# Performance work log

Hardware: AMD Instinct MI355X
Metric: run time of the kernel (lower is better)

## Reference

```python
import jax, jax.numpy as jnp
import numpy as np

B, N, L, D = 4, 2048, 12, 128  # batch, nodes, in_len, d_model


def _glorot(key, shape):
    fan_in = shape[0]
    return jax.random.normal(key, shape, dtype=jnp.float32) / jnp.sqrt(jnp.float32(fan_in))


def setup_inputs() -> dict:
    key = jax.random.key(0)
    ks = jax.random.split(key, 12)
    x = jax.random.normal(ks[0], (B, N, L, D), dtype=jnp.float32)
    adj = jax.random.uniform(ks[1], (N, N), dtype=jnp.float32)  # dense weighted adjacency
    # mlp2: Linear(L*D -> D)
    W_mlp2 = _glorot(ks[2], (L * D, D)); b_mlp2 = jnp.zeros((D,), jnp.float32)
    # GNN: three DenseSAGEConv layers (lin_rel on aggregated, lin_root on self)
    Wr1 = _glorot(ks[3], (D, D)); Wo1 = _glorot(ks[4], (D, D)); b1 = jnp.zeros((D,), jnp.float32)
    Wr2 = _glorot(ks[5], (D, D)); Wo2 = _glorot(ks[6], (D, D)); b2 = jnp.zeros((D,), jnp.float32)
    Wr3 = _glorot(ks[7], (D, D)); Wo3 = _glorot(ks[8], (D, D)); b3 = jnp.zeros((D,), jnp.float32)
    # mlp1: Linear(D -> L*D)
    W_mlp1 = _glorot(ks[9], (D, L * D)); b_mlp1 = jnp.zeros((L * D,), jnp.float32)
    return {"x": x, "adj": adj, "W_mlp2": W_mlp2, "b_mlp2": b_mlp2,
            "Wr1": Wr1, "Wo1": Wo1, "b1": b1,
            "Wr2": Wr2, "Wo2": Wo2, "b2": b2,
            "Wr3": Wr3, "Wo3": Wo3, "b3": b3,
            "W_mlp1": W_mlp1, "b_mlp1": b_mlp1}


def reference(x, adj, W_mlp2, b_mlp2, Wr1, Wo1, b1, Wr2, Wo2, b2, Wr3, Wo3, b3, W_mlp1, b_mlp1):
    b_, n_, l_, d_ = x.shape
    xf = x.reshape(b_, n_, l_ * d_)                      # 'b n l d -> b n (l d)'
    h = xf @ W_mlp2 + b_mlp2                             # mlp2: (B,N,D)
    deg = jnp.clip(adj.sum(axis=-1, keepdims=True), 1.0, None)  # (N,1)

    def sage(hin, Wr, Wo, bb):
        # mean neighbor aggregation: (adj @ h) / deg, then rel + root linear
        agg = jnp.einsum('mn,bnd->bmd', adj, hin) / deg
        return agg @ Wr + hin @ Wo + bb

    h = jax.nn.relu(sage(h, Wr1, Wo1, b1))
    h = jax.nn.relu(sage(h, Wr2, Wo2, b2))
    h = sage(h, Wr3, Wo3, b3)                            # gnn1_embed output (B,N,D)
    out = h @ W_mlp1 + b_mlp1                            # mlp1: (B,N,L*D)
    return out
```

## Files before the change

### kernel.cpp

```cpp
#include <hip/hip_runtime.h>

typedef __attribute__((ext_vector_type(8))) short short8;
typedef __attribute__((ext_vector_type(4))) short short4v;
typedef __attribute__((ext_vector_type(4))) float floatx4;

__device__ inline short to_bf16s(float f) {
    unsigned u = __builtin_bit_cast(unsigned, f);
    unsigned r = u + 0x7FFFu + ((u >> 16) & 1u);
    return (short)(r >> 16);
}

__device__ inline void dma16(const short* g, short* l) {
    __builtin_amdgcn_global_load_lds(
        (const __attribute__((address_space(1))) unsigned int*)(const void*)g,
        (__attribute__((address_space(3))) unsigned int*)(void*)l,
        16, 0, 0);
}

template <typename T> struct Ld8;
template <> struct Ld8<short> {
    static __device__ inline short8 load(const short* p) { return *(const short8*)p; }
};
template <> struct Ld8<float> {
    static __device__ inline short8 load(const float* p) {
        float4 f0 = *(const float4*)p;
        float4 f1 = *(const float4*)(p + 4);
        short8 r;
        r[0] = to_bf16s(f0.x); r[1] = to_bf16s(f0.y);
        r[2] = to_bf16s(f0.z); r[3] = to_bf16s(f0.w);
        r[4] = to_bf16s(f1.x); r[5] = to_bf16s(f1.y);
        r[6] = to_bf16s(f1.z); r[7] = to_bf16s(f1.w);
        return r;
    }
};

struct PrepArgs {
    const float* adj;
    const float* W2; const float* W1;
    const float* Wr0; const float* Wo0;
    const float* Wr1; const float* Wo1;
    const float* Wr2; const float* Wo2;
    short* adjS; short* W2T; short* W1T;
    short* BigB0; short* BigB1; short* BigB2;
};

__global__ __launch_bounds__(256) void prep(PrepArgs p) {
    int bid = blockIdx.x;
    if (bid < 2048) {
        const float* src = p.adj + (size_t)bid * 2048;
        float s = 0.f;
        for (int c = threadIdx.x; c < 2048; c += 256) s += src[c];
        __shared__ float red[256];
        red[threadIdx.x] = s;
        __syncthreads();
        for (int st = 128; st > 0; st >>= 1) {
            if (threadIdx.x < st) red[threadIdx.x] += red[threadIdx.x + st];
            __syncthreads();
        }
        float d = red[0];
        d = d < 1.f ? 1.f : d;
        float inv = 1.f / d;
        short* dst = p.adjS + (size_t)bid * 2048;
        for (int c = threadIdx.x; c < 2048; c += 256) dst[c] = to_bf16s(src[c] * inv);
        return;
    }
    int t = bid - 2048;
    __shared__ short tile[32][33];
    int tx = threadIdx.x & 31, ty0 = threadIdx.x >> 5;
    const float* in; int C_; int bx, by;
    short* outp; int outld, copies, copystride, outofs;
    if (t < 192) {
        bx = (t & 3) * 32; by = (t >> 2) * 32; in = p.W2; C_ = 128;
        outp = p.W2T; outld = 1536; copies = 1; copystride = 0; outofs = 0;
    } else if (t < 384) {
        int u = t - 192; bx = (u % 48) * 32; by = (u / 48) * 32; in = p.W1; C_ = 1536;
        outp = p.W1T; outld = 128; copies = 1; copystride = 0; outofs = 0;
    } else {
        int u = t - 384; int l = u / 32; int v = u % 32;
        const float* Wr[3] = {p.Wr0, p.Wr1, p.Wr2};
        const float* Wo[3] = {p.Wo0, p.Wo1, p.Wo2};
        short* BB[3] = {p.BigB0, p.BigB1, p.BigB2};
        outp = BB[l]; outld = 640; C_ = 128;
        if (v < 16) { in = Wr[l]; bx = (v & 3) * 32; by = (v >> 2) * 32;
                      copies = 4; copystride = 128; outofs = 0; }
        else { v -= 16; in = Wo[l]; bx = (v & 3) * 32; by = (v >> 2) * 32;
               copies = 1; copystride = 0; outofs = 512; }
    }
    for (int i = ty0; i < 32; i += 8)
        tile[i][tx] = to_bf16s(in[(size_t)(by + i) * C_ + bx + tx]);
    __syncthreads();
    for (int i = ty0; i < 32; i += 8) {
        short v = tile[tx][i];
        for (int c = 0; c < copies; ++c)
            outp[(size_t)(bx + i) * outld + (by + tx) + outofs + c * copystride] = v;
    }
}

#define LDSTR 72

template <typename TA, int RELU, int ROWMAP, int HTW>
__global__ __launch_bounds__(256) void gemmT(
    const TA* __restrict__ A, int lda,
    const short* __restrict__ B, int ldb, int kTiles,
    const float* __restrict__ bias,
    short* __restrict__ C, int ldc, int colofs,
    short* __restrict__ HT) {
    __shared__ __align__(16) short lds[2 * 96 * LDSTR];

    int tid = threadIdx.x;
    int blockM = blockIdx.x * 32;
    int blockN = blockIdx.y * 64;

    int srow = tid >> 3;
    int scol = (tid & 7) * 8;

    const TA* Abase = A + (size_t)blockM * lda;
    const short* Bbase = B + (size_t)blockN * ldb;

    short8 a0_  = Ld8<TA>::load(Abase + (size_t)srow * lda + scol);
    short8 b00_ = Ld8<short>::load(Bbase + (size_t)srow * ldb + scol);
    short8 b10_ = Ld8<short>::load(Bbase + (size_t)(srow + 32) * ldb + scol);
    short8 a1_  = Ld8<TA>::load(Abase + (size_t)srow * lda + 64 + scol);
    short8 b01_ = Ld8<short>::load(Bbase + (size_t)srow * ldb + 64 + scol);
    short8 b11_ = Ld8<short>::load(Bbase + (size_t)(srow + 32) * ldb + 64 + scol);

    floatx4 acc[2];
    #pragma unroll
    for (int j = 0; j < 2; ++j)
        #pragma unroll
        for (int r = 0; r < 4; ++r) acc[j][r] = 0.f;

    int lane = tid & 63;
    int w = tid >> 6;
    int wr = w >> 1, wc = w & 1;
    int quad = lane >> 4, l15 = lane & 15;

    short* buf0 = lds;
    short* buf1 = lds + 96 * LDSTR;

    for (int it = 0; it < kTiles; it += 2) {
        *(short8*)(buf0 + srow * LDSTR + scol) = a0_;
        *(short8*)(buf0 + (32 + srow) * LDSTR + scol) = b00_;
        *(short8*)(buf0 + (64 + srow) * LDSTR + scol) = b10_;
        asm volatile("s_waitcnt lgkmcnt(0)" ::: "memory");
        __builtin_amdgcn_s_barrier();
        if (it + 2 < kTiles) {
            int ko = (it + 2) * 64;
            a0_  = Ld8<TA>::load(Abase + (size_t)srow * lda + ko + scol);
            b00_ = Ld8<short>::load(Bbase + (size_t)srow * ldb + ko + scol);
            b10_ = Ld8<short>::load(Bbase + (size_t)(srow + 32) * ldb + ko + scol);
        }
        {
            const short* Arow = buf0 + (wr * 16 + l15) * LDSTR;
            const short* Brow = buf0 + (32 + wc * 32 + l15) * LDSTR;
            #pragma unroll
            for (int ks = 0; ks < 2; ++ks) {
                int kof = ks * 32 + quad * 8;
                short8 a0 = *(const short8*)(Arow + kof);
                short8 b0 = *(const short8*)(Brow + kof);
                short8 b1 = *(const short8*)(Brow + 16 * LDSTR + kof);
                acc[0] = __builtin_amdgcn_mfma_f32_16x16x32_bf16(a0, b0, acc[0], 0, 0, 0);
                acc[1] = __builtin_amdgcn_mfma_f32_16x16x32_bf16(a0, b1, acc[1], 0, 0, 0);
            }
        }
        *(short8*)(buf1 + srow * LDSTR + scol) = a1_;
        *(short8*)(buf1 + (32 + srow) * LDSTR + scol) = b01_;
        *(short8*)(buf1 + (64 + srow) * LDSTR + scol) = b11_;
        asm volatile("s_waitcnt lgkmcnt(0)" ::: "memory");
        __builtin_amdgcn_s_barrier();
        if (it + 3 < kTiles) {
            int ko = (it + 3) * 64;
            a1_  = Ld8<TA>::load(Abase + (size_t)srow * lda + ko + scol);
            b01_ = Ld8<short>::load(Bbase + (size_t)srow * ldb + ko + scol);
            b11_ = Ld8<short>::load(Bbase + (size_t)(srow + 32) * ldb + ko + scol);
        }
        {
            const short* Arow = buf1 + (wr * 16 + l15) * LDSTR;
            const short* Brow = buf1 + (32 + wc * 32 + l15) * LDSTR;
            #pragma unroll
            for (int ks = 0; ks < 2; ++ks) {
                int kof = ks * 32 + quad * 8;
                short8 a0 = *(const short8*)(Arow + kof);
                short8 b0 = *(const short8*)(Brow + kof);
                short8 b1 = *(const short8*)(Brow + 16 * LDSTR + kof);
                acc[0] = __builtin_amdgcn_mfma_f32_16x16x32_bf16(a0, b0, acc[0], 0, 0, 0);
                acc[1] = __builtin_amdgcn_mfma_f32_16x16x32_bf16(a0, b1, acc[1], 0, 0, 0);
            }
        }
    }

    #pragma unroll
    for (int tj = 0; tj < 2; ++tj) {
        int col = blockN + wc * 32 + tj * 16 + l15;
        float bv = bias[col];
        int m0 = blockM + wr * 16 + quad * 4;
        short4v pk;
        #pragma unroll
        for (int r = 0; r < 4; ++r) {
            int m = m0 + r;
            float xv = acc[tj][r] + bv;
            if (RELU) xv = xv > 0.f ? xv : 0.f;
            short v = to_bf16s(xv);
            pk[r] = v;
            int orow = ROWMAP ? (((m & 2047) << 2) | (m >> 11)) : m;
            C[(size_t)orow * ldc + col + colofs] = v;
            if (HTW && !ROWMAP) {
                HT[(size_t)((m & 3) * 128 + col) * 2048 + (m >> 2)] = v;
            }
        }
        if (HTW && ROWMAP) {
            int b = m0 >> 11, n0 = m0 & 2047;
            *(short4v*)(HT + (size_t)(b * 128 + col) * 2048 + n0) = pk;
        }
    }
}

__global__ __launch_bounds__(256) void gemmS(const short* __restrict__ A,
                                             const short* __restrict__ B,
                                             short* __restrict__ C) {
    __shared__ __align__(16) short lds3[3 * 12288];

    int tid = threadIdx.x;
    int kz = blockIdx.z * 512;

    int kswz = (((tid & 7) ^ ((tid >> 3) & 7))) * 8;
    const short* Ab = A + (size_t)(blockIdx.x * 64 + (tid >> 3)) * 2048 + kz + kswz;
    const short* Bb = B + (size_t)(blockIdx.y * 128 + (tid >> 3)) * 2048 + kz + kswz;

    floatx4 acc[2][4];
    #pragma unroll
    for (int i = 0; i < 2; ++i)
        #pragma unroll
        for (int j = 0; j < 4; ++j)
            #pragma unroll
            for (int r = 0; r < 4; ++r) acc[i][j][r] = 0.f;

    int lane = tid & 63;
    int w = tid >> 6;
    int wr = w >> 1, wc = w & 1;
    int quad = lane >> 4, l15 = lane & 15;

    auto stage = [&](int slot, int it) {
        short* As = lds3 + slot * 12288;
        short* Bs = As + 4096;
        const short* Ag = Ab + it * 64;
        const short* Bg = Bb + it * 64;
        dma16(Ag, As + tid * 8);
        dma16(Ag + (size_t)32 * 2048, As + tid * 8 + 2048);
        #pragma unroll
        for (int r = 0; r < 4; ++r)
            dma16(Bg + (size_t)r * 32 * 2048, Bs + tid * 8 + r * 2048);
    };

    stage(0, 0);
    stage(1, 1);

    int slot = 0;
    for (int it = 0; it < 8; ++it) {
        if (it < 7) asm volatile("s_waitcnt vmcnt(6)" ::: "memory");
        else        asm volatile("s_waitcnt vmcnt(0)" ::: "memory");
        __builtin_amdgcn_s_barrier();
        if (it + 2 < 8) {
            int s2 = slot + 2; if (s2 >= 3) s2 -= 3;
            stage(s2, it + 2);
        }
        const short* As = lds3 + slot * 12288;
        const short* Bs = As + 4096;
        #pragma unroll
        for (int ks = 0; ks < 2; ++ks) {
            int cswz = (((ks * 4 + quad) ^ (l15 & 7))) * 8;
            short8 af[2], bfr[4];
            #pragma unroll
            for (int i = 0; i < 2; ++i)
                af[i] = *(const short8*)(As + (wr * 32 + i * 16 + l15) * 64 + cswz);
            #pragma unroll
            for (int j = 0; j < 4; ++j)
                bfr[j] = *(const short8*)(Bs + (wc * 64 + j * 16 + l15) * 64 + cswz);
            #pragma unroll
            for (int i = 0; i < 2; ++i)
                #pragma unroll
                for (int j = 0; j < 4; ++j)
                    acc[i][j] = __builtin_amdgcn_mfma_f32_16x16x32_bf16(af[i], bfr[j], acc[i][j], 0, 0, 0);
        }
        slot = (slot + 1 == 3) ? 0 : slot + 1;
    }

    int colofs = blockIdx.z * 128;
    #pragma unroll
    for (int ti = 0; ti < 2; ++ti) {
        #pragma unroll
        for (int tj = 0; tj < 4; ++tj) {
            int j = blockIdx.y * 128 + wc * 64 + tj * 16 + l15;
            int jhi = j >> 7, jlo = j & 127;
            int row0 = blockIdx.x * 64 + wr * 32 + ti * 16 + quad * 4;
            #pragma unroll
            for (int r = 0; r < 4; ++r) {
                int m = row0 + r;
                C[(size_t)(m * 4 + jhi) * 640 + jlo + colofs] = to_bf16s(acc[ti][tj][r]);
            }
        }
    }
}

__global__ __launch_bounds__(256) void gemmL(
    const short* __restrict__ A, int lda,
    const short* __restrict__ B, int ldb,
    int kChunkIters, const float* __restrict__ bias,
    float* __restrict__ Cf, int ldc) {
    __shared__ __align__(16) short As[128 * 64];
    __shared__ __align__(16) short Bs[128 * 64];

    int tid = threadIdx.x;
    int blockM = blockIdx.x * 128;
    int blockN = blockIdx.y * 128;

    int kswz = (((tid & 7) ^ ((tid >> 3) & 7))) * 8;
    const short* Ab = A + (size_t)(blockM + (tid >> 3)) * lda + kswz;
    const short* Bb = B + (size_t)(blockN + (tid >> 3)) * ldb + kswz;
    short* Al = As + tid * 8;
    short* Bl = Bs + tid * 8;

    floatx4 acc[4][4];
    #pragma unroll
    for (int i = 0; i < 4; ++i)
        #pragma unroll
        for (int j = 0; j < 4; ++j)
            #pragma unroll
            for (int r = 0; r < 4; ++r) acc[i][j][r] = 0.f;

    int lane = tid & 63;
    int w = tid >> 6;
    int wr = w >> 1, wc = w & 1;
    int quad = lane >> 4, l15 = lane & 15;

    for (int it = 0; it < kChunkIters; ++it) {
        const short* Ag = Ab + it * 64;
        const short* Bg = Bb + it * 64;
        #pragma unroll
        for (int r = 0; r < 4; ++r) {
            dma16(Ag + (size_t)r * 32 * lda, Al + r * 2048);
            dma16(Bg + (size_t)r * 32 * ldb, Bl + r * 2048);
        }
        __syncthreads();
        #pragma unroll
        for (int ks = 0; ks < 2; ++ks) {
            int cswz = (((ks * 4 + quad) ^ (l15 & 7))) * 8;
            short8 af[4], bfr[4];
            #pragma unroll
            for (int i = 0; i < 4; ++i)
                af[i] = *(const short8*)(As + (wr * 64 + i * 16 + l15) * 64 + cswz);
            #pragma unroll
            for (int j = 0; j < 4; ++j)
                bfr[j] = *(const short8*)(Bs + (wc * 64 + j * 16 + l15) * 64 + cswz);
            #pragma unroll
            for (int i = 0; i < 4; ++i)
                #pragma unroll
                for (int j = 0; j < 4; ++j)
                    acc[i][j] = __builtin_amdgcn_mfma_f32_16x16x32_bf16(af[i], bfr[j], acc[i][j], 0, 0, 0);
        }
        __syncthreads();
    }

    #pragma unroll
    for (int ti = 0; ti < 4; ++ti) {
        #pragma unroll
        for (int tj = 0; tj < 4; ++tj) {
            int col = blockN + wc * 64 + tj * 16 + l15;
            float bv = bias[col];
            int row0 = blockM + wr * 64 + ti * 16 + quad * 4;
            #pragma unroll
            for (int r = 0; r < 4; ++r) {
                int mp = row0 + r;
                int orow = ((mp & 3) << 11) | (mp >> 2);
                Cf[(size_t)orow * ldc + col] = acc[ti][tj][r] + bv;
            }
        }
    }
}

extern "C" void kernel_launch(void* const* d_in, const int* in_sizes, int n_in,
                              void* d_out, int out_size, void* d_ws, size_t ws_size,
                              hipStream_t stream) {
    const float* x      = (const float*)d_in[0];
    const float* adj    = (const float*)d_in[1];
    const float* W_mlp2 = (const float*)d_in[2];
    const float* b_mlp2 = (const float*)d_in[3];
    const float* Wr1    = (const float*)d_in[4];
    const float* Wo1    = (const float*)d_in[5];
    const float* b1     = (const float*)d_in[6];
    const float* Wr2    = (const float*)d_in[7];
    const float* Wo2    = (const float*)d_in[8];
    const float* b2     = (const float*)d_in[9];
    const float* Wr3    = (const float*)d_in[10];
    const float* Wo3    = (const float*)d_in[11];
    const float* b3     = (const float*)d_in[12];
    const float* W_mlp1 = (const float*)d_in[13];
    const float* b_mlp1 = (const float*)d_in[14];
    float* out = (float*)d_out;

    char* ws = (char*)d_ws;
    size_t off = 0;
    auto alloc = [&](size_t bytes) -> char* {
        char* p = ws + off;
        off = (off + bytes + 255) & ~(size_t)255;
        return p;
    };
    short* W2T  = (short*)alloc(128 * 1536 * 2);
    short* W1T  = (short*)alloc(1536 * 128 * 2);
    short* BigB[3];
    for (int l = 0; l < 3; ++l) BigB[l] = (short*)alloc(128 * 640 * 2);
    short* adjS = (short*)alloc((size_t)2048 * 2048 * 2);
    short* big[4];
    for (int l = 0; l < 4; ++l) big[l] = (short*)alloc((size_t)8192 * 640 * 2);
    short* HT = (short*)alloc((size_t)512 * 2048 * 2);

    dim3 blk(256);

    PrepArgs pa{adj, W_mlp2, W_mlp1, Wr1, Wo1, Wr2, Wo2, Wr3, Wo3,
                adjS, W2T, W1T, BigB[0], BigB[1], BigB[2]};
    prep<<<2528, blk, 0, stream>>>(pa);

    gemmT<float, 0, 1, 1><<<dim3(256, 2), blk, 0, stream>>>(
        x, 1536, W2T, 1536, 24, b_mlp2, big[0], 640, 512, HT);

    for (int l = 0; l < 3; ++l) {
        gemmS<<<dim3(32, 4, 4), blk, 0, stream>>>(adjS, HT, big[l]);
        if (l == 0)
            gemmT<short, 1, 0, 1><<<dim3(256, 2), blk, 0, stream>>>(
                big[0], 640, BigB[0], 640, 10, b1, big[1], 640, 512, HT);
        else if (l == 1)
            gemmT<short, 1, 0, 1><<<dim3(256, 2), blk, 0, stream>>>(
                big[1], 640, BigB[1], 640, 10, b2, big[2], 640, 512, HT);
        else
            gemmT<short, 0, 0, 0><<<dim3(256, 2), blk, 0, stream>>>(
                big[2], 640, BigB[2], 640, 10, b3, big[3], 640, 512, nullptr);
    }

    gemmL<<<dim3(64, 12), blk, 0, stream>>>(big[3] + 512, 640, W1T, 128, 2, b_mlp1, out, 1536);
}
```

Measured before the change: 212.5 us.

## Fuse adjacency normalization into first GEMM launch and widen gemmS to 8 waves

The adjacency row-normalization is moved out of the prep kernel into a combined launch that also runs the first mlp2 GEMM, so the two independent jobs share one grid. Weight transposes stay in a smaller prep kernel. Separately, gemmS now runs 512 threads per block, so each wave owns one 16-row A fragment instead of two. This halves per-wave accumulators and spreads the DMA loads across more threads, raising parallelism at the same tile size. The cost is less register reuse of B fragments per wave and more LDS reads per MFMA.

```diff
diff --git a/kernel.cpp b/kernel.cpp
--- a/kernel.cpp
+++ b/kernel.cpp
@@ -44,27 +44,8 @@
     short* BigB0; short* BigB1; short* BigB2;
 };
 
-__global__ __launch_bounds__(256) void prep(PrepArgs p) {
-    int bid = blockIdx.x;
-    if (bid < 2048) {
-        const float* src = p.adj + (size_t)bid * 2048;
-        float s = 0.f;
-        for (int c = threadIdx.x; c < 2048; c += 256) s += src[c];
-        __shared__ float red[256];
-        red[threadIdx.x] = s;
-        __syncthreads();
-        for (int st = 128; st > 0; st >>= 1) {
-            if (threadIdx.x < st) red[threadIdx.x] += red[threadIdx.x + st];
-            __syncthreads();
-        }
-        float d = red[0];
-        d = d < 1.f ? 1.f : d;
-        float inv = 1.f / d;
-        short* dst = p.adjS + (size_t)bid * 2048;
-        for (int c = threadIdx.x; c < 2048; c += 256) dst[c] = to_bf16s(src[c] * inv);
-        return;
-    }
-    int t = bid - 2048;
+__global__ __launch_bounds__(256) void prepW(PrepArgs p) {
+    int t = blockIdx.x;
     __shared__ short tile[32][33];
     int tx = threadIdx.x & 31, ty0 = threadIdx.x >> 5;
     const float* in; int C_; int bx, by;
@@ -99,17 +80,16 @@
 #define LDSTR 72
 
 template <typename TA, int RELU, int ROWMAP, int HTW>
-__global__ __launch_bounds__(256) void gemmT(
+__device__ __forceinline__ void dev_gemmT(
+    short* lds, int bidx, int bidy,
     const TA* __restrict__ A, int lda,
     const short* __restrict__ B, int ldb, int kTiles,
     const float* __restrict__ bias,
     short* __restrict__ C, int ldc, int colofs,
     short* __restrict__ HT) {
-    __shared__ __align__(16) short lds[2 * 96 * LDSTR];
-
     int tid = threadIdx.x;
-    int blockM = blockIdx.x * 32;
-    int blockN = blockIdx.y * 64;
+    int blockM = bidx * 32;
+    int blockN = bidy * 64;
 
     int srow = tid >> 3;
     int scol = (tid & 7) * 8;
@@ -215,7 +195,50 @@
     }
 }
 
-__global__ __launch_bounds__(256) void gemmS(const short* __restrict__ A,
+template <typename TA, int RELU, int ROWMAP, int HTW>
+__global__ __launch_bounds__(256) void gemmT(
+    const TA* __restrict__ A, int lda,
+    const short* __restrict__ B, int ldb, int kTiles,
+    const float* __restrict__ bias,
+    short* __restrict__ C, int ldc, int colofs,
+    short* __restrict__ HT) {
+    __shared__ __align__(16) short lds[2 * 96 * LDSTR];
+    dev_gemmT<TA, RELU, ROWMAP, HTW>(lds, blockIdx.x, blockIdx.y,
+                                     A, lda, B, ldb, kTiles, bias, C, ldc, colofs, HT);
+}
+
+__global__ __launch_bounds__(256) void fusedA(PrepArgs p,
+                                              const float* __restrict__ x,
+                                              const float* __restrict__ b_mlp2,
+                                              short* __restrict__ big0,
+                                              short* __restrict__ HT) {
+    __shared__ __align__(16) short lds[2 * 96 * LDSTR];
+    int bid = blockIdx.x;
+    if (bid < 512) {
+        dev_gemmT<float, 0, 1, 1>(lds, bid & 255, bid >> 8,
+                                  x, 1536, p.W2T, 1536, 24, b_mlp2,
+                                  big0, 640, 512, HT);
+        return;
+    }
+    int row = bid - 512;
+    const float* src = p.adj + (size_t)row * 2048;
+    float s = 0.f;
+    for (int c = threadIdx.x; c < 2048; c += 256) s += src[c];
+    float* red = (float*)lds;
+    red[threadIdx.x] = s;
+    __syncthreads();
+    for (int st = 128; st > 0; st >>= 1) {
+        if (threadIdx.x < st) red[threadIdx.x] += red[threadIdx.x + st];
+        __syncthreads();
+    }
+    float d = red[0];
+    d = d < 1.f ? 1.f : d;
+    float inv = 1.f / d;
+    short* dst = p.adjS + (size_t)row * 2048;
+    for (int c = threadIdx.x; c < 2048; c += 256) dst[c] = to_bf16s(src[c] * inv);
+}
+
+__global__ __launch_bounds__(512) void gemmS(const short* __restrict__ A,
                                              const short* __restrict__ B,
                                              short* __restrict__ C) {
     __shared__ __align__(16) short lds3[3 * 12288];
@@ -227,17 +250,15 @@
     const short* Ab = A + (size_t)(blockIdx.x * 64 + (tid >> 3)) * 2048 + kz + kswz;
     const short* Bb = B + (size_t)(blockIdx.y * 128 + (tid >> 3)) * 2048 + kz + kswz;
 
-    floatx4 acc[2][4];
-    #pragma unroll
-    for (int i = 0; i < 2; ++i)
-        #pragma unroll
-        for (int j = 0; j < 4; ++j)
-            #pragma unroll
-            for (int r = 0; r < 4; ++r) acc[i][j][r] = 0.f;
+    floatx4 acc[4];
+    #pragma unroll
+    for (int j = 0; j < 4; ++j)
+        #pragma unroll
+        for (int r = 0; r < 4; ++r) acc[j][r] = 0.f;
 
     int lane = tid & 63;
     int w = tid >> 6;
-    int wr = w >> 1, wc = w & 1;
+    int wr = w & 3, wc = w >> 2;
     int quad = lane >> 4, l15 = lane & 15;
 
     auto stage = [&](int slot, int it) {
@@ -246,10 +267,8 @@
         const short* Ag = Ab + it * 64;
         const short* Bg = Bb + it * 64;
         dma16(Ag, As + tid * 8);
-        dma16(Ag + (size_t)32 * 2048, As + tid * 8 + 2048);
-        #pragma unroll
-        for (int r = 0; r < 4; ++r)
-            dma16(Bg + (size_t)r * 32 * 2048, Bs + tid * 8 + r * 2048);
+        dma16(Bg, Bs + tid * 8);
+        dma16(Bg + (size_t)64 * 2048, Bs + tid * 8 + 4096);
     };
 
     stage(0, 0);
@@ -257,7 +276,7 @@
 
     int slot = 0;
     for (int it = 0; it < 8; ++it) {
-        if (it < 7) asm volatile("s_waitcnt vmcnt(6)" ::: "memory");
+        if (it < 7) asm volatile("s_waitcnt vmcnt(3)" ::: "memory");
         else        asm volatile("s_waitcnt vmcnt(0)" ::: "memory");
         __builtin_amdgcn_s_barrier();
         if (it + 2 < 8) {
@@ -269,35 +288,28 @@
         #pragma unroll
         for (int ks = 0; ks < 2; ++ks) {
             int cswz = (((ks * 4 + quad) ^ (l15 & 7))) * 8;
-            short8 af[2], bfr[4];
-            #pragma unroll
-            for (int i = 0; i < 2; ++i)
-                af[i] = *(const short8*)(As + (wr * 32 + i * 16 + l15) * 64 + cswz);
+            short8 af = *(const short8*)(As + (wr * 16 + l15) * 64 + cswz);
+            short8 bfr[4];
             #pragma unroll
             for (int j = 0; j < 4; ++j)
                 bfr[j] = *(const short8*)(Bs + (wc * 64 + j * 16 + l15) * 64 + cswz);
             #pragma unroll
-            for (int i = 0; i < 2; ++i)
-                #pragma unroll
-                for (int j = 0; j < 4; ++j)
-                    acc[i][j] = __builtin_amdgcn_mfma_f32_16x16x32_bf16(af[i], bfr[j], acc[i][j], 0, 0, 0);
+            for (int j = 0; j < 4; ++j)
+                acc[j] = __builtin_amdgcn_mfma_f32_16x16x32_bf16(af, bfr[j], acc[j], 0, 0, 0);
         }
         slot = (slot + 1 == 3) ? 0 : slot + 1;
     }
 
     int colofs = blockIdx.z * 128;
     #pragma unroll
-    for (int ti = 0; ti < 2; ++ti) {
-        #pragma unroll
-        for (int tj = 0; tj < 4; ++tj) {
-            int j = blockIdx.y * 128 + wc * 64 + tj * 16 + l15;
-            int jhi = j >> 7, jlo = j & 127;
-            int row0 = blockIdx.x * 64 + wr * 32 + ti * 16 + quad * 4;
-            #pragma unroll
-            for (int r = 0; r < 4; ++r) {
-                int m = row0 + r;
-                C[(size_t)(m * 4 + jhi) * 640 + jlo + colofs] = to_bf16s(acc[ti][tj][r]);
-            }
+    for (int tj = 0; tj < 4; ++tj) {
+        int j = blockIdx.y * 128 + wc * 64 + tj * 16 + l15;
+        int jhi = j >> 7, jlo = j & 127;
+        int row0 = blockIdx.x * 64 + wr * 16 + quad * 4;
+        #pragma unroll
+        for (int r = 0; r < 4; ++r) {
+            int m = row0 + r;
+            C[(size_t)(m * 4 + jhi) * 640 + jlo + colofs] = to_bf16s(acc[tj][r]);
         }
     }
 }
@@ -418,13 +430,12 @@
 
     PrepArgs pa{adj, W_mlp2, W_mlp1, Wr1, Wo1, Wr2, Wo2, Wr3, Wo3,
                 adjS, W2T, W1T, BigB[0], BigB[1], BigB[2]};
-    prep<<<2528, blk, 0, stream>>>(pa);
-
-    gemmT<float, 0, 1, 1><<<dim3(256, 2), blk, 0, stream>>>(
-        x, 1536, W2T, 1536, 24, b_mlp2, big[0], 640, 512, HT);
+    prepW<<<480, blk, 0, stream>>>(pa);
+
+    fusedA<<<2560, blk, 0, stream>>>(pa, x, b_mlp2, big[0], HT);
 
     for (int l = 0; l < 3; ++l) {
-        gemmS<<<dim3(32, 4, 4), blk, 0, stream>>>(adjS, HT, big[l]);
+        gemmS<<<dim3(32, 4, 4), dim3(512), 0, stream>>>(adjS, HT, big[l]);
         if (l == 0)
             gemmT<short, 1, 0, 1><<<dim3(256, 2), blk, 0, stream>>>(
                 big[0], 640, BigB[0], 640, 10, b1, big[1], 640, 512, HT);
```

After: 211.7 us. About the same (-0.3%).
